# Kernel optimization log

Measured on AMD Instinct MI355X. Metric: run time of the kernel, lower is better.

Reference implementation:

```python
import jax, jax.numpy as jnp
import numpy as np

NL, NS, NE = 16, 256, 100   # nlatent, nspatial, n_embd
B, P, T = 2, 2, 12


def _xavier(key, shape):
    # torch xavier_uniform: fan_in = shape[1]*prod(rest), fan_out = shape[0]*prod(rest)
    rf = int(np.prod(shape[2:])) if len(shape) > 2 else 1
    fan_in, fan_out = shape[1] * rf, shape[0] * rf
    b = float(np.sqrt(6.0 / (fan_in + fan_out)))
    return jax.random.uniform(key, shape, jnp.float32, -b, b)


def setup_inputs() -> dict:
    key = jax.random.key(0)
    ks = jax.random.split(key, 8)
    x = jax.random.normal(ks[0], (B, P, T, NL, NS), jnp.float32)
    K = _xavier(ks[1], (NS, NS, NL))
    Q = _xavier(ks[2], (NS, NS, NL))
    V = _xavier(ks[3], (NS, NS, NL))
    Aoo = jnp.ones((NS, NS), jnp.float32)
    # Ann is initialized to zeros in the module; use nonzero values so the
    # clamped geometric recurrence over time is actually exercised.
    Ann = jax.random.uniform(ks[4], (NE,), jnp.float32, -0.9, 0.9)
    Aon = _xavier(ks[5], (NS, NS, NE))
    Ano = _xavier(ks[6], (NS, NS, NE))
    w = jnp.ones((NS,), jnp.float32) / NS
    return {"x": x, "K": K, "Q": Q, "V": V, "Aoo": Aoo,
            "Ann": Ann, "Aon": Aon, "Ano": Ano, "w": w}


def reference(x, K, Q, V, Aoo, Ann, Aon, Ano, w):
    # kvt[B,p,T,X,Y] = sum_{x,c} Q[Y,x,c] K[X,x,c] x[B,p,T,c,x]
    kvt = jnp.einsum('Yxc,Xxc,BpTcx->BpTXY', Q, K, x)
    Aon_c = jnp.clip(Aon, -1.0, 1.0)
    Ano_c = jnp.clip(Ano, -1.0, 1.0)

    # t = T-1 term (elementwise Aoo) and t = T-2 term
    h = Aoo[None, None, None] * kvt[:, :, -1:]
    h = h + jnp.einsum('xyn,XYn,BpTXY->BpTxy', Aon_c, Ano_c, kvt[:, :, -2:-1])

    nT = x.shape[2]
    # Ann sequence used in the loop: A_2 = Ann (raw), A_{j+1} = clip(A_j * Ann)
    def step(a, _):
        return jnp.clip(a * Ann, -1.0, 1.0), a
    _, A_seq = jax.lax.scan(step, Ann, None, length=nT - 2)  # [T-2, n], A_seq[j-2]=A_j

    # loop index j=2..T-1 touches time slice t = T-1-j, i.e. t = T-3 .. 0
    s = jnp.einsum('XYn,BpJXY->BpJn', Ano_c, kvt[:, :, :nT - 2])  # J = t in 0..T-3
    A_t = A_seq[::-1]                       # align A_j with time index t = T-1-j
    s2 = jnp.einsum('Jn,BpJn->Bpn', A_t, s)
    h = h + jnp.einsum('xyn,Bpn->Bpxy', Aon_c, s2)[:, :, None]  # [B,p,1,x,y]

    q = jnp.einsum('Xxc,Bpcx->BpcX', V, x[:, :, -1])
    y = jnp.einsum('x,BpcX,BpTXx->BpTc', w, q, h)  # [B,p,1,c]
    return y
```

## Files before the change

### kernel.cpp

```cpp
#include <hip/hip_runtime.h>
#include <hip/hip_fp16.h>


using f32x4 = __attribute__((ext_vector_type(4))) float;
using half8 = __attribute__((ext_vector_type(8))) _Float16;
using half4 = __attribute__((ext_vector_type(4))) _Float16;

#define KVT_STRIDE 3145728ull
#define KS 4

__device__ inline float clip1(float v) { return fminf(fmaxf(v, -1.f), 1.f); }

__device__ inline half8 mul8(uint4 a, uint4 b) {
    half8 x = __builtin_bit_cast(half8, a);
    half8 y = __builtin_bit_cast(half8, b);
    return x * y;
}

__device__ __forceinline__ void gl_lds16(const void* g, void* l) {
    __builtin_amdgcn_global_load_lds(
        (const __attribute__((address_space(1))) void*)g,
        (__attribute__((address_space(3))) void*)l, 16, 0, 0);
}

__global__ void prep_kernel(const float* __restrict__ K, const float* __restrict__ Q,
                            const float* __restrict__ xin,
                            const float* __restrict__ Aon, const float* __restrict__ wv,
                            const float* __restrict__ V,
                            __half* __restrict__ Kh, __half* __restrict__ Qh,
                            __half* __restrict__ u_t,
                            float* __restrict__ W2p, float* __restrict__ R)
{
    int b = blockIdx.x, t = threadIdx.x;
    if (b < 2048) {
        bool isK = (b < 1024);
        int bb = isK ? b : b - 1024;
        int i = bb * 1024 + t * 4;
        const float4 f = ((const float4*)(isK ? K : Q))[i >> 2];
        half4 v = { (_Float16)f.x, (_Float16)f.y, (_Float16)f.z, (_Float16)f.w };
        *(half4*)((isK ? Kh : Qh) + i) = v;
    } else if (b < 2096) {
        int bt = b - 2048;
        const float* src = xin + (size_t)bt * 4096;
        int xx = t;
        half8 lo, hi;
        #pragma unroll
        for (int c = 0; c < 8; ++c)  lo[c] = (_Float16)src[c * 256 + xx];
        #pragma unroll
        for (int c = 0; c < 8; ++c)  hi[c] = (_Float16)src[(c + 8) * 256 + xx];
        half8* dst = (half8*)(u_t + (size_t)bt * 4096 + xx * 16);
        dst[0] = lo; dst[1] = hi;
    } else if (b < 2608) {
        int idx = b - 2096;
        int X = idx >> 1, h = idx & 1;
        int g = h * 2 + (t >> 7), n = t & 127;
        if (n < 100) {
            const float* base = Aon + (size_t)X * 25600 + (size_t)g * 6400 + n;
            float acc = 0.f;
            for (int bb = 0; bb < 64; ++bb)
                acc += wv[g * 64 + bb] * clip1(__builtin_nontemporal_load(base + (size_t)bb * 100));
            W2p[((size_t)g * 256 + X) * 100 + n] = acc;
        }
    } else {
        __shared__ float vrow[4096];
        int X = b - 2608;
        {
            const float4* src = (const float4*)(V + (size_t)X * 4096);
            float4* dst = (float4*)vrow;
            for (int i = t; i < 1024; i += 256) dst[i] = src[i];
        }
        __syncthreads();
        int bp = t >> 6, c = (t >> 2) & 15, g = t & 3;
        const float* xl = xin + ((size_t)(bp * 12) + 11) * 4096 + c * 256;
        float p = 0.f;
        #pragma unroll 4
        for (int x = g * 64; x < g * 64 + 64; ++x)
            p += xl[x] * vrow[x * 16 + c];
        p += __shfl_xor(p, 1);
        p += __shfl_xor(p, 2);
        if (g == 0) R[((size_t)bp * 256 + X) * 16 + c] = p;
    }
}

__global__ __launch_bounds__(256, 4) void gemm_kvt(
    const __half* __restrict__ Kh, const __half* __restrict__ Qh,
    const __half* __restrict__ u_t, __half* __restrict__ kvtp)
{
    __shared__ __half As[2][128][32];
    __shared__ __half Bs[2][128][32];
    __shared__ __half u_s[1024];

    int bid = blockIdx.x;
    int work = (bid & 7) * 96 + (bid >> 3);
    int kc = work / 192;
    int rem = work - kc * 192;
    int tile = rem / 48;
    int bt = rem - tile * 48;
    int Xb = (tile >> 1) * 128, Yb = (tile & 1) * 128;
    int kbase = kc * 1024;

    int tid = threadIdx.x;
    if (tid < 128)
        *(uint4*)&u_s[tid * 8] = *(const uint4*)(u_t + (size_t)bt * 4096 + kbase + tid * 8);
    __syncthreads();

    int wave = tid >> 6, lane = tid & 63;

    int arow = tid >> 1;
    int apair = (tid & 1) * 2;
    const __half* gA = Kh + (size_t)(Xb + arow) * 4096 + kbase + apair * 8;
    int aswz = (arow >> 1) & 3;
    int asb0 = ((apair + 0) ^ aswz) << 4;
    int asb1 = ((apair + 1) ^ aswz) << 4;

    int srow = lane >> 2;
    int sk = ((lane & 3) ^ ((srow >> 1) & 3)) << 3;
    const __half* gB = Qh + (size_t)(Yb + wave * 16 + srow) * 4096 + kbase + sk;

    int wr = (wave >> 1) * 64, wc = (wave & 1) * 64;
    int lrow = lane & 15, kg = lane >> 4;
    int fb = (kg * 16) ^ (((lrow >> 1) & 3) << 4);

    f32x4 acc[4][4];
    f32x4 zero = {0.f, 0.f, 0.f, 0.f};
    #pragma unroll
    for (int m = 0; m < 4; ++m)
        #pragma unroll
        for (int n = 0; n < 4; ++n) acc[m][n] = zero;

    #define ISSUE_B(s, buf)                                                    \
        do {                                                                   \
            _Pragma("unroll")                                                  \
            for (int i_ = 0; i_ < 2; ++i_)                                     \
                gl_lds16(gB + (size_t)(i_ * 64) * 4096 + (s) * 32,             \
                         &Bs[buf][i_ * 64 + wave * 16][0]);                    \
        } while (0)

    #define WRITE_A(s, r0, r1, buf)                                            \
        do {                                                                   \
            uint4 uv0 = *(const uint4*)&u_s[(s) * 32 + apair * 8];             \
            uint4 uv1 = *(const uint4*)&u_s[(s) * 32 + apair * 8 + 8];         \
            *(half8*)((char*)&As[buf][arow][0] + asb0) = mul8(r0, uv0);        \
            *(half8*)((char*)&As[buf][arow][0] + asb1) = mul8(r1, uv1);        \
        } while (0)

    #define COMPUTE(cur)                                                       \
        do {                                                                   \
            half8 af[4], bf[4];                                                \
            _Pragma("unroll")                                                  \
            for (int m = 0; m < 4; ++m)                                        \
                af[m] = *(const half8*)((const char*)&As[cur][wr + m * 16 + lrow][0] + fb); \
            _Pragma("unroll")                                                  \
            for (int n = 0; n < 4; ++n)                                        \
                bf[n] = *(const half8*)((const char*)&Bs[cur][wc + n * 16 + lrow][0] + fb); \
            _Pragma("unroll")                                                  \
            for (int m = 0; m < 4; ++m)                                        \
                _Pragma("unroll")                                              \
                for (int n = 0; n < 4; ++n)                                    \
                    acc[m][n] = __builtin_amdgcn_mfma_f32_16x16x32_f16(af[m], bf[n], acc[m][n], 0, 0, 0); \
        } while (0)

    #define STEP(s, c0, c1, i0, i1, cur)                                       \
        do {                                                                   \
            if ((s) < 31) asm volatile("s_waitcnt vmcnt(4) lgkmcnt(0)" ::: "memory"); \
            else          asm volatile("s_waitcnt vmcnt(0) lgkmcnt(0)" ::: "memory"); \
            __builtin_amdgcn_s_barrier();                                      \
            __builtin_amdgcn_sched_barrier(0);                                 \
            COMPUTE(cur);                                                      \
            asm volatile("s_waitcnt lgkmcnt(0)" ::: "memory");                 \
            __builtin_amdgcn_s_barrier();                                      \
            __builtin_amdgcn_sched_barrier(0);                                 \
            if ((s) + 2 < 32) {                                                \
                const __half* a_ = gA + ((s) + 2) * 32;                        \
                i0 = *(const uint4*)a_;                                        \
                i1 = *(const uint4*)(a_ + 8);                                  \
                ISSUE_B((s) + 2, cur);                                         \
            }                                                                  \
            if ((s) + 1 < 32) WRITE_A((s) + 1, c0, c1, (cur) ^ 1);             \
        } while (0)

    uint4 aP0, aP1, aC0, aC1;
    aP0 = *(const uint4*)gA;
    aP1 = *(const uint4*)(gA + 8);
    ISSUE_B(0, 0);
    aC0 = *(const uint4*)(gA + 32);
    aC1 = *(const uint4*)(gA + 40);
    ISSUE_B(1, 1);
    WRITE_A(0, aP0, aP1, 0);

    #pragma unroll
    for (int s = 0; s < 32; s += 2) {
        STEP(s,     aC0, aC1, aP0, aP1, 0);
        STEP(s + 1, aP0, aP1, aC0, aC1, 1);
    }
    #undef STEP
    #undef COMPUTE
    #undef WRITE_A
    #undef ISSUE_B

    __half* outp = kvtp + (size_t)kc * KVT_STRIDE + (size_t)bt * 65536;
    int row0 = Xb + wr + kg * 4;
    int col0 = Yb + wc + lrow;
    #pragma unroll
    for (int m = 0; m < 4; ++m)
        #pragma unroll
        for (int n = 0; n < 4; ++n)
            #pragma unroll
            for (int rr = 0; rr < 4; ++rr)
                outp[(size_t)(row0 + m * 16 + rr) * 256 + col0 + n * 16] =
                    __float2half(acc[m][n][rr]);
}

__global__ __launch_bounds__(256) void s_partial(const float* __restrict__ Ano,
                                                 const __half* __restrict__ kvtp,
                                                 float* __restrict__ Sp)
{
    __shared__ float ano_f[12864];
    __shared__ float kvt_s[44][128];
    int cb = blockIdx.x;
    int k0 = cb * 128;
    int tid = threadIdx.x;

    {
        const f32x4* src = (const f32x4*)(Ano + (size_t)k0 * 100);
        f32x4* dst = (f32x4*)ano_f;
        for (int i = tid; i < 3200; i += 256) {
            f32x4 f = __builtin_nontemporal_load(src + i);
            f.x = clip1(f.x); f.y = clip1(f.y); f.z = clip1(f.z); f.w = clip1(f.w);
            dst[i] = f;
        }
    }
    {
        for (int idx = tid; idx < 5632; idx += 256) {
            int rI = idx >> 7, k = idx & 127;
            int bpr = rI / 11, Jr = rI - bpr * 11;
            size_t off = (size_t)(bpr * 12 + Jr) * 65536 + k0 + k;
            float v = 0.f;
            #pragma unroll
            for (int c = 0; c < KS; ++c)
                v += __half2float(kvtp[(size_t)c * KVT_STRIDE + off]);
            kvt_s[rI][k] = v;
        }
    }
    __syncthreads();

    int lane = tid & 63;
    int bp = tid >> 6;
    bool has2 = lane < 36;
    float acc0[11], acc1[11];
    #pragma unroll
    for (int J = 0; J < 11; ++J) { acc0[J] = 0.f; acc1[J] = 0.f; }

    for (int k = 0; k < 128; k += 4) {
        f32x4 kv[11];
        #pragma unroll
        for (int J = 0; J < 11; ++J)
            kv[J] = *(const f32x4*)&kvt_s[bp * 11 + J][k];
        #pragma unroll
        for (int kk = 0; kk < 4; ++kk) {
            float a0 = ano_f[(k + kk) * 100 + lane];
            float a1r = ano_f[(k + kk) * 100 + 64 + lane];
            float a1 = has2 ? a1r : 0.f;
            #pragma unroll
            for (int J = 0; J < 11; ++J) {
                acc0[J] += kv[J][kk] * a0;
                acc1[J] += kv[J][kk] * a1;
            }
        }
    }
    float* outb = Sp + ((size_t)cb * 4 + bp) * 1100;
    #pragma unroll
    for (int J = 0; J < 11; ++J) {
        outb[J * 100 + lane] = acc0[J];
        if (has2) outb[J * 100 + 64 + lane] = acc1[J];
    }
}

__global__ void reduce_s(const float* __restrict__ Sp, float* __restrict__ Sq,
                         float* __restrict__ out)
{
    int bid = blockIdx.x;
    int t = threadIdx.x;
    if (bid == 0 && t < 64) out[t] = 0.f;
    int qq = bid & 3, idx = bid >> 2;
    int bp = idx / 11, J = idx - bp * 11;
    if (t >= 100) return;
    float acc = 0.f;
    for (int c = qq * 128; c < qq * 128 + 128; ++c)
        acc += Sp[((size_t)c * 4 + bp) * 1100 + J * 100 + t];
    Sq[(size_t)(qq * 44 + idx) * 100 + t] = acc;
}

__global__ __launch_bounds__(256) void hw_kernel(const float* __restrict__ Aoo,
                                                 const float* __restrict__ wv,
                                                 const __half* __restrict__ kvtp,
                                                 const float* __restrict__ W2p,
                                                 const float* __restrict__ Sq,
                                                 const float* __restrict__ Ann,
                                                 const float* __restrict__ R,
                                                 float* __restrict__ out)
{
    __shared__ float yp[4][16];
    __shared__ float c2s[128];
    int bp = blockIdx.x >> 6, Xg = blockIdx.x & 63;
    int tid = threadIdx.x;

    if (tid < 128) {
        int n = tid;
        float r = 0.f;
        if (n < 100) {
            float S[11];
            #pragma unroll
            for (int J = 0; J < 11; ++J) {
                float s = 0.f;
                #pragma unroll
                for (int qq = 0; qq < 4; ++qq)
                    s += Sq[(size_t)(qq * 44 + bp * 11 + J) * 100 + n];
                S[J] = s;
            }
            float a = Ann[n];
            float seq[10];
            float v = a;
            seq[0] = v;
            #pragma unroll
            for (int s2 = 1; s2 < 10; ++s2) { v = clip1(v * a); seq[s2] = v; }
            r = S[10];
            #pragma unroll
            for (int J = 0; J < 10; ++J)
                r += seq[9 - J] * S[J];
        }
        c2s[n] = r;
    }
    __syncthreads();

    int wave = tid >> 6, lane = tid & 63;
    int X = Xg * 4 + wave;
    size_t base = (size_t)(bp * 12 + 11) * 65536 + (size_t)X * 256;
    const float* ao = Aoo + (size_t)X * 256;
    float red = 0.f;
    #pragma unroll
    for (int qq = 0; qq < 4; ++qq) {
        int xx = qq * 64 + lane;
        float kvv = 0.f;
        #pragma unroll
        for (int c = 0; c < KS; ++c)
            kvv += __half2float(kvtp[(size_t)c * KVT_STRIDE + base + xx]);
        red += wv[xx] * ao[xx] * kvv;
    }
    float w2a = 0.f, w2b = 0.f;
    #pragma unroll
    for (int g = 0; g < 4; ++g) {
        w2a += W2p[((size_t)g * 256 + X) * 100 + lane];
        if (lane < 36) w2b += W2p[((size_t)g * 256 + X) * 100 + 64 + lane];
    }
    red += c2s[lane] * w2a;
    if (lane < 36)
        red += c2s[64 + lane] * w2b;
    #pragma unroll
    for (int off = 32; off; off >>= 1) red += __shfl_xor(red, off);
    if (lane < 16) yp[wave][lane] = red * R[((size_t)bp * 256 + X) * 16 + lane];
    __syncthreads();
    if (tid < 16) {
        float s = yp[0][tid] + yp[1][tid] + yp[2][tid] + yp[3][tid];
        atomicAdd(&out[bp * 16 + tid], s);
    }
}

extern "C" void kernel_launch(void* const* d_in, const int* in_sizes, int n_in,
                              void* d_out, int out_size, void* d_ws, size_t ws_size,
                              hipStream_t stream)
{
    const float* x   = (const float*)d_in[0];
    const float* K   = (const float*)d_in[1];
    const float* Q   = (const float*)d_in[2];
    const float* V   = (const float*)d_in[3];
    const float* Aoo = (const float*)d_in[4];
    const float* Ann = (const float*)d_in[5];
    const float* Aon = (const float*)d_in[6];
    const float* Ano = (const float*)d_in[7];
    const float* wv  = (const float*)d_in[8];
    float* out = (float*)d_out;

    char* ws = (char*)d_ws;
    const size_t o_Qh   = 0;
    const size_t o_Kh   = o_Qh + (size_t)2 * 1024 * 1024;
    const size_t o_ut   = o_Kh + (size_t)2 * 1024 * 1024;
    const size_t o_kvtp = o_ut + (size_t)512 * 1024;
    const size_t o_Sp   = o_kvtp + (size_t)KS * KVT_STRIDE * 2;
    const size_t o_Sq   = o_Sp + (size_t)512 * 4400 * 4;
    const size_t o_W2   = o_Sq + (size_t)17600 * 4 + 64;
    const size_t o_R    = o_W2 + (size_t)102400 * 4;

    __half* Qh  = (__half*)(ws + o_Qh);
    __half* Kh  = (__half*)(ws + o_Kh);
    __half* u_t = (__half*)(ws + o_ut);
    __half* kvtp = (__half*)(ws + o_kvtp);
    float* Sp   = (float*)(ws + o_Sp);
    float* Sq   = (float*)(ws + o_Sq);
    float* W2p  = (float*)(ws + o_W2);
    float* R    = (float*)(ws + o_R);

    hipLaunchKernelGGL(prep_kernel, dim3(2864), dim3(256), 0, stream,
                       K, Q, x, Aon, wv, V, Kh, Qh, u_t, W2p, R);
    hipLaunchKernelGGL(gemm_kvt,    dim3(768),  dim3(256), 0, stream, Kh, Qh, u_t, kvtp);
    hipLaunchKernelGGL(s_partial,   dim3(512),  dim3(256), 0, stream, Ano, kvtp, Sp);
    hipLaunchKernelGGL(reduce_s,    dim3(176),  dim3(128), 0, stream, Sp, Sq, out);
    hipLaunchKernelGGL(hw_kernel,   dim3(256),  dim3(256), 0, stream,
                       Aoo, wv, kvtp, W2p, Sq, Ann, R, out);
}
```

Baseline: 104.2 us.

## Move W2p and R computation into merged mid kernel, transpose Ano in LDS

```diff
diff --git a/kernel.cpp b/kernel.cpp
--- a/kernel.cpp
+++ b/kernel.cpp
@@ -25,22 +25,28 @@
 
 __global__ void prep_kernel(const float* __restrict__ K, const float* __restrict__ Q,
                             const float* __restrict__ xin,
-                            const float* __restrict__ Aon, const float* __restrict__ wv,
-                            const float* __restrict__ V,
                             __half* __restrict__ Kh, __half* __restrict__ Qh,
-                            __half* __restrict__ u_t,
-                            float* __restrict__ W2p, float* __restrict__ R)
+                            __half* __restrict__ u_t)
 {
     int b = blockIdx.x, t = threadIdx.x;
-    if (b < 2048) {
-        bool isK = (b < 1024);
-        int bb = isK ? b : b - 1024;
-        int i = bb * 1024 + t * 4;
-        const float4 f = ((const float4*)(isK ? K : Q))[i >> 2];
-        half4 v = { (_Float16)f.x, (_Float16)f.y, (_Float16)f.z, (_Float16)f.w };
-        *(half4*)((isK ? Kh : Qh) + i) = v;
-    } else if (b < 2096) {
-        int bt = b - 2048;
+    if (b < 512) {
+        bool isK = (b < 256);
+        int bb = isK ? b : b - 256;
+        size_t base = (size_t)bb * 4096 + t * 16;
+        const f32x4* src = (const f32x4*)((isK ? K : Q) + base);
+        __half* dst = (isK ? Kh : Qh) + base;
+        #pragma unroll
+        for (int j = 0; j < 2; ++j) {
+            f32x4 v0 = src[j * 2], v1 = src[j * 2 + 1];
+            half8 h;
+            h[0] = (_Float16)v0.x; h[1] = (_Float16)v0.y;
+            h[2] = (_Float16)v0.z; h[3] = (_Float16)v0.w;
+            h[4] = (_Float16)v1.x; h[5] = (_Float16)v1.y;
+            h[6] = (_Float16)v1.z; h[7] = (_Float16)v1.w;
+            *(half8*)(dst + j * 8) = h;
+        }
+    } else {
+        int bt = b - 512;
         const float* src = xin + (size_t)bt * 4096;
         int xx = t;
         half8 lo, hi;
@@ -50,35 +56,6 @@
         for (int c = 0; c < 8; ++c)  hi[c] = (_Float16)src[(c + 8) * 256 + xx];
         half8* dst = (half8*)(u_t + (size_t)bt * 4096 + xx * 16);
         dst[0] = lo; dst[1] = hi;
-    } else if (b < 2608) {
-        int idx = b - 2096;
-        int X = idx >> 1, h = idx & 1;
-        int g = h * 2 + (t >> 7), n = t & 127;
-        if (n < 100) {
-            const float* base = Aon + (size_t)X * 25600 + (size_t)g * 6400 + n;
-            float acc = 0.f;
-            for (int bb = 0; bb < 64; ++bb)
-                acc += wv[g * 64 + bb] * clip1(__builtin_nontemporal_load(base + (size_t)bb * 100));
-            W2p[((size_t)g * 256 + X) * 100 + n] = acc;
-        }
-    } else {
-        __shared__ float vrow[4096];
-        int X = b - 2608;
-        {
-            const float4* src = (const float4*)(V + (size_t)X * 4096);
-            float4* dst = (float4*)vrow;
-            for (int i = t; i < 1024; i += 256) dst[i] = src[i];
-        }
-        __syncthreads();
-        int bp = t >> 6, c = (t >> 2) & 15, g = t & 3;
-        const float* xl = xin + ((size_t)(bp * 12) + 11) * 4096 + c * 256;
-        float p = 0.f;
-        #pragma unroll 4
-        for (int x = g * 64; x < g * 64 + 64; ++x)
-            p += xl[x] * vrow[x * 16 + c];
-        p += __shfl_xor(p, 1);
-        p += __shfl_xor(p, 2);
-        if (g == 0) R[((size_t)bp * 256 + X) * 16 + c] = p;
     }
 }
 
@@ -211,68 +188,111 @@
                     __float2half(acc[m][n][rr]);
 }
 
-__global__ __launch_bounds__(256) void s_partial(const float* __restrict__ Ano,
-                                                 const __half* __restrict__ kvtp,
-                                                 float* __restrict__ Sp)
-{
-    __shared__ float ano_f[12864];
-    __shared__ float kvt_s[44][128];
-    int cb = blockIdx.x;
-    int k0 = cb * 128;
-    int tid = threadIdx.x;
-
-    {
-        const f32x4* src = (const f32x4*)(Ano + (size_t)k0 * 100);
-        f32x4* dst = (f32x4*)ano_f;
-        for (int i = tid; i < 3200; i += 256) {
-            f32x4 f = __builtin_nontemporal_load(src + i);
-            f.x = clip1(f.x); f.y = clip1(f.y); f.z = clip1(f.z); f.w = clip1(f.w);
-            dst[i] = f;
-        }
-    }
-    {
-        for (int idx = tid; idx < 5632; idx += 256) {
-            int rI = idx >> 7, k = idx & 127;
-            int bpr = rI / 11, Jr = rI - bpr * 11;
-            size_t off = (size_t)(bpr * 12 + Jr) * 65536 + k0 + k;
-            float v = 0.f;
-            #pragma unroll
-            for (int c = 0; c < KS; ++c)
-                v += __half2float(kvtp[(size_t)c * KVT_STRIDE + off]);
-            kvt_s[rI][k] = v;
-        }
-    }
-    __syncthreads();
-
-    int lane = tid & 63;
-    int bp = tid >> 6;
-    bool has2 = lane < 36;
-    float acc0[11], acc1[11];
-    #pragma unroll
-    for (int J = 0; J < 11; ++J) { acc0[J] = 0.f; acc1[J] = 0.f; }
-
-    for (int k = 0; k < 128; k += 4) {
-        f32x4 kv[11];
-        #pragma unroll
-        for (int J = 0; J < 11; ++J)
-            kv[J] = *(const f32x4*)&kvt_s[bp * 11 + J][k];
-        #pragma unroll
-        for (int kk = 0; kk < 4; ++kk) {
-            float a0 = ano_f[(k + kk) * 100 + lane];
-            float a1r = ano_f[(k + kk) * 100 + 64 + lane];
-            float a1 = has2 ? a1r : 0.f;
-            #pragma unroll
-            for (int J = 0; J < 11; ++J) {
-                acc0[J] += kv[J][kk] * a0;
-                acc1[J] += kv[J][kk] * a1;
+__global__ __launch_bounds__(256) void mid_kernel(
+    const float* __restrict__ Ano, const __half* __restrict__ kvtp,
+    const float* __restrict__ V, const float* __restrict__ xin,
+    const float* __restrict__ Aon, const float* __restrict__ wv,
+    float* __restrict__ Sp, float* __restrict__ R, float* __restrict__ W2p)
+{
+    __shared__ __align__(16) char smem[75328];
+    int b = blockIdx.x, tid = threadIdx.x;
+
+    if (b < 512) {
+        float* anoT = (float*)smem;
+        float (*kvt_s)[128] = (float(*)[128])(smem + 52800);
+        int cb = b;
+        int k0 = cb * 128;
+
+        {
+            const f32x4* src = (const f32x4*)(Ano + (size_t)k0 * 100);
+            for (int i = tid; i < 3200; i += 256) {
+                f32x4 f = __builtin_nontemporal_load(src + i);
+                int e = i * 4;
+                int k = e / 100;
+                int n = e - k * 100;
+                #pragma unroll
+                for (int j = 0; j < 4; ++j) {
+                    int nn = n + j, kk2 = k;
+                    if (nn >= 100) { nn -= 100; ++kk2; }
+                    anoT[nn * 132 + kk2] = clip1(f[j]);
+                }
             }
         }
-    }
-    float* outb = Sp + ((size_t)cb * 4 + bp) * 1100;
-    #pragma unroll
-    for (int J = 0; J < 11; ++J) {
-        outb[J * 100 + lane] = acc0[J];
-        if (has2) outb[J * 100 + 64 + lane] = acc1[J];
+        {
+            for (int idx = tid; idx < 5632; idx += 256) {
+                int rI = idx >> 7, k = idx & 127;
+                int bpr = rI / 11, Jr = rI - bpr * 11;
+                size_t off = (size_t)(bpr * 12 + Jr) * 65536 + k0 + k;
+                float v = 0.f;
+                #pragma unroll
+                for (int c = 0; c < KS; ++c)
+                    v += __half2float(kvtp[(size_t)c * KVT_STRIDE + off]);
+                kvt_s[rI][k] = v;
+            }
+        }
+        __syncthreads();
+
+        int lane = tid & 63;
+        int bp = tid >> 6;
+        bool has2 = lane < 36;
+        float acc0[11], acc1[11];
+        #pragma unroll
+        for (int J = 0; J < 11; ++J) { acc0[J] = 0.f; acc1[J] = 0.f; }
+
+        const float* a0p = anoT + lane * 132;
+        const float* a1p = anoT + (64 + lane) * 132;
+        for (int k = 0; k < 128; k += 4) {
+            f32x4 kv[11];
+            #pragma unroll
+            for (int J = 0; J < 11; ++J)
+                kv[J] = *(const f32x4*)&kvt_s[bp * 11 + J][k];
+            f32x4 a0v = *(const f32x4*)(a0p + k);
+            f32x4 a1v = {0.f, 0.f, 0.f, 0.f};
+            if (has2) a1v = *(const f32x4*)(a1p + k);
+            #pragma unroll
+            for (int kk = 0; kk < 4; ++kk) {
+                #pragma unroll
+                for (int J = 0; J < 11; ++J) {
+                    acc0[J] += kv[J][kk] * a0v[kk];
+                    acc1[J] += kv[J][kk] * a1v[kk];
+                }
+            }
+        }
+        float* outb = Sp + ((size_t)cb * 4 + bp) * 1100;
+        #pragma unroll
+        for (int J = 0; J < 11; ++J) {
+            outb[J * 100 + lane] = acc0[J];
+            if (has2) outb[J * 100 + 64 + lane] = acc1[J];
+        }
+    } else if (b < 768) {
+        float* vrow = (float*)smem;
+        int X = b - 512;
+        {
+            const float4* src = (const float4*)(V + (size_t)X * 4096);
+            float4* dst = (float4*)vrow;
+            for (int i = tid; i < 1024; i += 256) dst[i] = src[i];
+        }
+        __syncthreads();
+        int bp = tid >> 6, c = (tid >> 2) & 15, g = tid & 3;
+        const float* xl = xin + ((size_t)(bp * 12) + 11) * 4096 + c * 256;
+        float p = 0.f;
+        #pragma unroll 4
+        for (int x = g * 64; x < g * 64 + 64; ++x)
+            p += xl[x] * vrow[x * 16 + c];
+        p += __shfl_xor(p, 1);
+        p += __shfl_xor(p, 2);
+        if (g == 0) R[((size_t)bp * 256 + X) * 16 + c] = p;
+    } else {
+        int idx = b - 768;
+        int X = idx >> 1, h = idx & 1;
+        int g = h * 2 + (tid >> 7), n = tid & 127;
+        if (n < 100) {
+            const float* base = Aon + (size_t)X * 25600 + (size_t)g * 6400 + n;
+            float acc = 0.f;
+            for (int bb = 0; bb < 64; ++bb)
+                acc += wv[g * 64 + bb] * clip1(__builtin_nontemporal_load(base + (size_t)bb * 100));
+            W2p[((size_t)g * 256 + X) * 100 + n] = acc;
+        }
     }
 }
 
@@ -400,10 +420,11 @@
     float* W2p  = (float*)(ws + o_W2);
     float* R    = (float*)(ws + o_R);
 
-    hipLaunchKernelGGL(prep_kernel, dim3(2864), dim3(256), 0, stream,
-                       K, Q, x, Aon, wv, V, Kh, Qh, u_t, W2p, R);
+    hipLaunchKernelGGL(prep_kernel, dim3(560),  dim3(256), 0, stream,
+                       K, Q, x, Kh, Qh, u_t);
     hipLaunchKernelGGL(gemm_kvt,    dim3(768),  dim3(256), 0, stream, Kh, Qh, u_t, kvtp);
-    hipLaunchKernelGGL(s_partial,   dim3(512),  dim3(256), 0, stream, Ano, kvtp, Sp);
+    hipLaunchKernelGGL(mid_kernel,  dim3(1280), dim3(256), 0, stream,
+                       Ano, kvtp, V, x, Aon, wv, Sp, R, W2p);
     hipLaunchKernelGGL(reduce_s,    dim3(176),  dim3(128), 0, stream, Sp, Sq, out);
     hipLaunchKernelGGL(hw_kernel,   dim3(256),  dim3(256), 0, stream,
                        Aoo, wv, kvtp, W2p, Sq, Ann, R, out);
```

Measured after the change: 98.88 us. 5.1% less time.
